# Performance work log

Hardware: AMD Instinct MI355X
Metric: run time of the kernel (lower is better)

The kernel has to match this reference:

```python
import jax, jax.numpy as jnp
import numpy as np

BS, SEQ, D_MODEL = 4, 1024, 4096
N_Q_HEADS, N_KV_HEADS, D_K, D_V = 32, 8, 128, 128
ROPE_BASE = 10000.0


def _rotate_half(x):
    x1, x2 = jnp.split(x, 2, axis=-1)
    return jnp.concatenate([-x2, x1], axis=-1)


def _apply_rope(x, pos0):
    # x: [bs, heads, seq, d]; positions pos0 .. pos0+seq-1
    d = x.shape[-1]
    seq = x.shape[2]
    inv_freq = 1.0 / (ROPE_BASE ** (jnp.arange(0, d, 2, dtype=jnp.float32) / d))  # [d/2]
    pos = (pos0 + jnp.arange(seq)).astype(jnp.float32)  # [seq]
    ang = pos[:, None] * inv_freq[None, :]  # [seq, d/2]
    cos = jnp.concatenate([jnp.cos(ang), jnp.cos(ang)], axis=-1)  # [seq, d]
    sin = jnp.concatenate([jnp.sin(ang), jnp.sin(ang)], axis=-1)
    return x * cos[None, None] + _rotate_half(x) * sin[None, None]


def setup_inputs() -> dict:
    key = jax.random.key(0)
    ks = jax.random.split(key, 8)
    w_scale = 0.02  # keep logits in a sane range (original uses raw normal init)
    return {
        "query": jax.random.normal(ks[0], (BS, SEQ, D_MODEL), dtype=jnp.float32),
        "key": jax.random.normal(ks[1], (BS, SEQ, D_MODEL), dtype=jnp.float32),
        "value": jax.random.normal(ks[2], (BS, SEQ, D_MODEL), dtype=jnp.float32),
        "mask": jnp.zeros((BS, SEQ, SEQ), dtype=jnp.float32),
        "wq": jax.random.normal(ks[3], (D_MODEL, N_Q_HEADS * D_K), dtype=jnp.float32) * w_scale,
        "wk": jax.random.normal(ks[4], (D_MODEL, N_KV_HEADS * D_K), dtype=jnp.float32) * w_scale,
        "wv": jax.random.normal(ks[5], (D_MODEL, N_KV_HEADS * D_V), dtype=jnp.float32) * w_scale,
        "wo": jax.random.normal(ks[6], (N_Q_HEADS * D_V, D_MODEL), dtype=jnp.float32) * w_scale,
        "curr_seq_pos": 0,
    }


def reference(query, key, value, mask, wq, wk, wv, wo, curr_seq_pos):
    bs, sq, _ = query.shape
    n_groups = N_Q_HEADS // N_KV_HEADS
    # projections -> [bs, heads, seq, d]
    q = (query @ wq).reshape(bs, sq, N_Q_HEADS, D_K).transpose((0, 2, 1, 3))
    sk = key.shape[1]
    k = (key @ wk).reshape(bs, sk, N_KV_HEADS, 1, D_K)
    k = jnp.repeat(k, n_groups, axis=3).reshape(bs, sk, N_Q_HEADS, D_K).transpose((0, 2, 1, 3))
    v = (value @ wv).reshape(bs, sk, N_KV_HEADS, 1, D_V)
    v = jnp.repeat(v, n_groups, axis=3).reshape(bs, sk, N_Q_HEADS, D_V).transpose((0, 2, 1, 3))
    scale = jnp.sqrt(jnp.float32(D_K))
    q = _apply_rope(q, curr_seq_pos)
    k = _apply_rope(k, curr_seq_pos)
    # [bs, h, sq, sk]
    raw = jnp.einsum("bhqd,bhkd->bhqk", q, k) / scale
    masked = raw + mask[:bs, None, curr_seq_pos:curr_seq_pos + sq, :sk]
    attn = jax.nn.softmax(masked, axis=-1)
    out = jnp.einsum("bhqk,bhkd->bhqd", attn, v)
    out = out.transpose((0, 2, 1, 3)).reshape(bs, sq, N_Q_HEADS * D_V)
    return out @ wo
```

## Files before the change

### kernel.cpp

```cpp
#include <hip/hip_runtime.h>


using ushort = unsigned short;
typedef __attribute__((ext_vector_type(8))) short short8;
typedef __attribute__((ext_vector_type(4))) short short4v;
typedef __attribute__((ext_vector_type(4))) float f32x4;
typedef __attribute__((ext_vector_type(4))) unsigned int uint4v;

__device__ __forceinline__ ushort f2bf(float x) {
  unsigned int u = __float_as_uint(x);
  u += 0x7FFFu + ((u >> 16) & 1u);
  return (ushort)(u >> 16);
}
__device__ __forceinline__ float bf2f(ushort h) {
  return __uint_as_float(((unsigned int)h) << 16);
}
__device__ __forceinline__ unsigned int cvt_pk_bf16(float lo, float hi) {
  unsigned int r;
  asm("v_cvt_pk_bf16_f32 %0, %1, %2" : "=v"(r) : "v"(lo), "v"(hi));
  return r;
}

__device__ __forceinline__ void async_copy16(const void* g, void* l) {
  __builtin_amdgcn_global_load_lds((const __attribute__((address_space(1))) void*)g,
                                   (__attribute__((address_space(3))) void*)l, 16, 0, 0);
}

__global__ __launch_bounds__(256)
void cvt_f32_bf16(const float* __restrict__ in, ushort* __restrict__ out, int n4) {
  const int i = blockIdx.x * 256 + threadIdx.x;
  if (i < n4) {
    const float4 f = ((const float4*)in)[i];
    short4v v;
    v[0] = (short)f2bf(f.x); v[1] = (short)f2bf(f.y);
    v[2] = (short)f2bf(f.z); v[3] = (short)f2bf(f.w);
    ((short4v*)out)[i] = v;
  }
}

__global__ __launch_bounds__(256)
void transpose_cvt(const float* __restrict__ B, ushort* __restrict__ Bt, int N) {
  __shared__ ushort t[64][72];
  const int n0 = blockIdx.x * 64, k0 = blockIdx.y * 64;
  const int tid = threadIdx.x;
  const int r = tid >> 3, c8 = (tid & 7) * 8;
#pragma unroll
  for (int p = 0; p < 2; p++) {
    const float* src = B + (size_t)(k0 + r + p * 32) * N + n0 + c8;
    const float4 f0 = *(const float4*)src;
    const float4 f1 = *(const float4*)(src + 4);
    ushort* d = &t[r + p * 32][c8];
    d[0] = f2bf(f0.x); d[1] = f2bf(f0.y); d[2] = f2bf(f0.z); d[3] = f2bf(f0.w);
    d[4] = f2bf(f1.x); d[5] = f2bf(f1.y); d[6] = f2bf(f1.z); d[7] = f2bf(f1.w);
  }
  __syncthreads();
#pragma unroll
  for (int p = 0; p < 2; p++) {
    const int n = r + p * 32;
    short8 o;
#pragma unroll
    for (int j = 0; j < 8; j++) o[j] = (short)t[c8 + j][n];
    *(short8*)(Bt + (size_t)(n0 + n) * 4096 + k0 + c8) = o;
  }
}

template <int MODE, bool AF32>
__global__ __launch_bounds__(256, 2)
void gemm_bt(const float* __restrict__ Af, const float* __restrict__ A2f,
             const ushort* __restrict__ Abf, const ushort* __restrict__ Bt,
             ushort* __restrict__ C, ushort* __restrict__ C2,
             float* __restrict__ Cf, const int* __restrict__ posp,
             int N, float scale) {
  constexpr int K = 4096;
  __shared__ alignas(16) ushort As[128 * 32];
  __shared__ alignas(16) ushort Bs[128 * 32];
  const int tid = threadIdx.x;
  const int wave = tid >> 6, lane = tid & 63;
  const int quad = lane >> 4, l16 = lane & 15;
  const int m0 = blockIdx.y * 128, n0 = blockIdx.x * 128;
  const int wm = (wave & 1) * 64, wn2 = (wave >> 1) * 32;

  const size_t aoff = (size_t)(m0 + wave * 16 + (lane >> 2)) * K + (lane & 3) * 8;
  const float* gAf = nullptr;
  const ushort* gAb = nullptr;
  if constexpr (AF32) {
    const float* Ause = Af;
    if constexpr (MODE == 4) {
      if (n0 >= 1024) Ause = A2f;
    }
    gAf = Ause + aoff;
  } else {
    gAb = Abf + aoff;
  }
  const ushort* gB = Bt + (size_t)(n0 + wave * 16 + (lane >> 2)) * K + (lane & 3) * 8;
  ushort* lA = As + wave * 512;
  ushort* lB = Bs + wave * 512;
  constexpr size_t rstep = (size_t)64 * K;

  f32x4 acc[4][4] = {};

  for (int kt = 0; kt < K; kt += 32) {
    if constexpr (AF32) {
      const float4 a0 = *(const float4*)(gAf + kt);
      const float4 a1 = *(const float4*)(gAf + kt + 4);
      const float4 b0 = *(const float4*)(gAf + rstep + kt);
      const float4 b1 = *(const float4*)(gAf + rstep + kt + 4);
      uint4v v0, v1;
      v0[0] = cvt_pk_bf16(a0.x, a0.y); v0[1] = cvt_pk_bf16(a0.z, a0.w);
      v0[2] = cvt_pk_bf16(a1.x, a1.y); v0[3] = cvt_pk_bf16(a1.z, a1.w);
      v1[0] = cvt_pk_bf16(b0.x, b0.y); v1[1] = cvt_pk_bf16(b0.z, b0.w);
      v1[2] = cvt_pk_bf16(b1.x, b1.y); v1[3] = cvt_pk_bf16(b1.z, b1.w);
      *(uint4v*)(lA + lane * 8) = v0;
      *(uint4v*)(lA + 2048 + lane * 8) = v1;
    } else {
      async_copy16(gAb + kt, lA);
      async_copy16(gAb + rstep + kt, lA + 2048);
    }
    async_copy16(gB + kt, lB);
    async_copy16(gB + rstep + kt, lB + 2048);
    __syncthreads();
    short8 af[4], bfrag[4];
#pragma unroll
    for (int i = 0; i < 4; i++) {
      af[i] = *(const short8*)(As + (wm + i * 16 + l16) * 32 + quad * 8);
      bfrag[i] = *(const short8*)(
          Bs + (wn2 + (i & 1) * 16 + (i >> 1) * 64 + l16) * 32 + quad * 8);
    }
#pragma unroll
    for (int i = 0; i < 4; i++)
#pragma unroll
      for (int j = 0; j < 4; j++)
        acc[i][j] = __builtin_amdgcn_mfma_f32_16x16x32_bf16(af[i], bfrag[j],
                                                            acc[i][j], 0, 0, 0);
    __syncthreads();
  }

  if constexpr (MODE == 0) {
#pragma unroll
    for (int i = 0; i < 4; i++)
#pragma unroll
      for (int j = 0; j < 4; j++) {
        const int n = n0 + wn2 + (j & 1) * 16 + (j >> 1) * 64 + l16;
        const int mb = m0 + wm + i * 16 + quad * 4;
#pragma unroll
        for (int r = 0; r < 4; r++)
          Cf[(size_t)(mb + r) * N + n] = acc[i][j][r] * scale;
      }
  } else {
    const bool kv_v = (MODE == 4) && (n0 >= 1024);
    if (!kv_v) {
      const int pos0 = posp[0];
      const int h = (MODE == 1) ? (n0 >> 7) : (n0 >> 7);
      const int NH = (MODE == 1) ? 32 : 8;
      constexpr float lgbase = -0.20762050593045983f;
      float invf[2];
      invf[0] = exp2f((float)(wn2 + l16) * lgbase);
      invf[1] = exp2f((float)(wn2 + 16 + l16) * lgbase);
#pragma unroll
      for (int i = 0; i < 4; i++) {
#pragma unroll
        for (int r = 0; r < 4; r++) {
          const int m = m0 + wm + i * 16 + quad * 4 + r;
          const int s = m & 1023, bb = m >> 10;
          const float p = (float)(s + pos0);
          ushort* row = C + (((size_t)bb * NH + h) * 1024 + s) * 128;
#pragma unroll
          for (int jj = 0; jj < 2; jj++) {
            float sn, cs;
            sincosf(p * invf[jj], &sn, &cs);
            const float x1 = acc[i][jj][r] * scale;
            const float x2 = acc[i][jj + 2][r] * scale;
            const int dlo = wn2 + jj * 16 + l16;
            row[dlo] = f2bf(x1 * cs - x2 * sn);
            row[dlo + 64] = f2bf(x2 * cs + x1 * sn);
          }
        }
      }
    } else {
      const int hh = (n0 - 1024) >> 7;
#pragma unroll
      for (int i = 0; i < 4; i++)
#pragma unroll
        for (int j = 0; j < 4; j++) {
          const int d = wn2 + (j & 1) * 16 + (j >> 1) * 64 + l16;
          const int mb = m0 + wm + i * 16 + quad * 4;
#pragma unroll
          for (int r = 0; r < 4; r++) {
            const int m = mb + r;
            const int bb = m >> 10, s = m & 1023;
            C2[(((size_t)bb * 8 + hh) * 128 + d) * 1024 + s] = f2bf(acc[i][j][r]);
          }
        }
    }
  }
}

__global__ __launch_bounds__(256, 2)
void attn_kernel(const ushort* __restrict__ Qh, const ushort* __restrict__ Kh,
                 const ushort* __restrict__ Vt, const ushort* __restrict__ Mk,
                 ushort* __restrict__ Oh) {
  __shared__ alignas(16) ushort smem[36864];
  ushort* const Ks0 = smem;
  ushort* const Ks1 = smem + 8192;
  ushort* const Vs0 = smem + 16384;
  ushort* const Vs1 = smem + 24576;
  ushort* const Ps = smem + 32768;
  ushort* const Qtmp = smem + 16384;

  int bid = (blockIdx.z * 32 + blockIdx.y) * 16 + blockIdx.x;
  bid = (bid & 7) * 256 + (bid >> 3);
  const int b = bid >> 9, h = (bid >> 4) & 31;
  const int q0 = (bid & 15) * 64;
  const int hkv = h >> 2;
  const int tid = threadIdx.x;
  const int wave = tid >> 6, lane = tid & 63;
  const int quad = lane >> 4, l16 = lane & 15;
  const int vr = lane >> 3;
  const int vkc = (lane & 7) ^ (vr & 7);

  const ushort* Qg = Qh + (((size_t)b * 32 + h) * 1024 + q0) * 128;
  const ushort* Kg = Kh + ((size_t)b * 8 + hkv) * (size_t)(1024 * 128);
  const ushort* Vg = Vt + ((size_t)b * 8 + hkv) * (size_t)(128 * 1024);
  const ushort* Mg = Mk + ((size_t)b * 1024 + q0) * 1024;

#pragma unroll
  for (int c = 0; c < 4; c++) {
    const int i = wave * 4 + c;
    const int row = i * 4 + quad;
    const int kc = l16 ^ (c * 4 + quad);
    async_copy16(Qg + (size_t)row * 128 + kc * 8, Qtmp + i * 512);
  }
#pragma unroll
  for (int c = 0; c < 4; c++) {
    const int i = wave * 4 + c;
    const int row = i * 4 + quad;
    const int kc = l16 ^ (c * 4 + quad);
    async_copy16(Kg + (size_t)row * 128 + kc * 8, Ks0 + i * 512);
  }
  __asm__ volatile("s_waitcnt vmcnt(0)" ::: "memory");
  short8 qreg[4];
#pragma unroll
  for (int ks = 0; ks < 4; ks++)
    qreg[ks] = *(const short8*)(Qtmp + (size_t)(wave * 16 + l16) * 128 +
                                (((ks * 4 + quad) ^ l16) * 8));
  __syncthreads();
#pragma unroll
  for (int c = 0; c < 4; c++) {
    const int i = wave * 4 + c;
    async_copy16(Vg + (size_t)(i * 8 + vr) * 1024 + vkc * 8, Vs0 + i * 512);
  }

  float m_i[4], l_p[4];
#pragma unroll
  for (int r = 0; r < 4; r++) { m_i[r] = -1e30f; l_p[r] = 0.0f; }
  f32x4 acc[8] = {};

  ushort* const PW = Ps + wave * 1024;

  for (int kt = 0; kt < 1024; kt += 64) {
    const int it = kt >> 6;
    ushort* const Kc = (it & 1) ? Ks1 : Ks0;
    ushort* const Vc = (it & 1) ? Vs1 : Vs0;
    ushort* const Kn = (it & 1) ? Ks0 : Ks1;
    ushort* const Vn = (it & 1) ? Vs0 : Vs1;
    __syncthreads();

    ushort mr[4][4];
#pragma unroll
    for (int nt = 0; nt < 4; nt++)
#pragma unroll
      for (int r = 0; r < 4; r++)
        mr[nt][r] = Mg[(size_t)(wave * 16 + quad * 4 + r) * 1024 +
                       kt + nt * 16 + l16];

    f32x4 s[4] = {};
    __builtin_amdgcn_s_setprio(1);
#pragma unroll
    for (int ks = 0; ks < 4; ks++) {
      const int ko = ((ks * 4 + quad) ^ l16) * 8;
#pragma unroll
      for (int nt = 0; nt < 4; nt++) {
        const short8 bk = *(const short8*)(Kc + (size_t)(nt * 16 + l16) * 128 + ko);
        s[nt] = __builtin_amdgcn_mfma_f32_16x16x32_bf16(qreg[ks], bk, s[nt], 0, 0, 0);
      }
    }
    __builtin_amdgcn_s_setprio(0);

    if (kt < 960) {
#pragma unroll
      for (int c = 0; c < 4; c++) {
        const int i = wave * 4 + c;
        const int row = i * 4 + quad;
        const int kc = l16 ^ (c * 4 + quad);
        async_copy16(Kg + (size_t)(kt + 64 + row) * 128 + kc * 8, Kn + i * 512);
      }
#pragma unroll
      for (int c = 0; c < 4; c++) {
        const int i = wave * 4 + c;
        async_copy16(Vg + (size_t)(i * 8 + vr) * 1024 + kt + 64 + vkc * 8, Vn + i * 512);
      }
    }

#pragma unroll
    for (int nt = 0; nt < 4; nt++)
#pragma unroll
      for (int r = 0; r < 4; r++) s[nt][r] += bf2f(mr[nt][r]);

    float mx[4];
    int need = 0;
#pragma unroll
    for (int r = 0; r < 4; r++) {
      float v = fmaxf(fmaxf(s[0][r], s[1][r]), fmaxf(s[2][r], s[3][r]));
#pragma unroll
      for (int off = 1; off < 16; off <<= 1) v = fmaxf(v, __shfl_xor(v, off));
      mx[r] = v;
      need |= (v > m_i[r] + 8.0f) ? 1 : 0;
    }
    if (__any(need)) {
#pragma unroll
      for (int r = 0; r < 4; r++) {
        const float mnew = fmaxf(m_i[r], mx[r]);
        const float al = __expf(m_i[r] - mnew);
        m_i[r] = mnew;
        l_p[r] *= al;
#pragma unroll
        for (int dt = 0; dt < 8; dt++) acc[dt][r] *= al;
      }
    }

#pragma unroll
    for (int r = 0; r < 4; r++) {
      const int prow = quad * 4 + r;
      const int key8 = ((prow >> 1) & 7) * 8;
      const float p0 = __expf(s[0][r] - m_i[r]);
      const float p1 = __expf(s[1][r] - m_i[r]);
      const float p2 = __expf(s[2][r] - m_i[r]);
      const float p3 = __expf(s[3][r] - m_i[r]);
      l_p[r] += (p0 + p1) + (p2 + p3);
      const unsigned int u01 = cvt_pk_bf16(p0, p1);
      const unsigned int u23 = cvt_pk_bf16(p2, p3);
      ushort* row = PW + prow * 64;
      row[l16 ^ key8] = (ushort)u01;
      row[(16 + l16) ^ key8] = (ushort)(u01 >> 16);
      row[(32 + l16) ^ key8] = (ushort)u23;
      row[(48 + l16) ^ key8] = (ushort)(u23 >> 16);
    }
    __asm__ volatile("s_waitcnt lgkmcnt(0)" ::: "memory");

    __builtin_amdgcn_s_setprio(1);
#pragma unroll
    for (int kk = 0; kk < 2; kk++) {
      const int pslot = ((kk * 4 + quad) ^ (l16 >> 1)) * 8;
      const short8 ap = *(const short8*)(PW + (size_t)l16 * 64 + pslot);
#pragma unroll
      for (int dt = 0; dt < 8; dt++) {
        const int vo = ((kk * 4 + quad) ^ (l16 & 7)) * 8;
        const short8 bv = *(const short8*)(Vc + (size_t)(dt * 16 + l16) * 64 + vo);
        acc[dt] = __builtin_amdgcn_mfma_f32_16x16x32_bf16(ap, bv, acc[dt], 0, 0, 0);
      }
    }
    __builtin_amdgcn_s_setprio(0);
  }

  ushort* Og = Oh + ((size_t)b * 1024 + q0 + wave * 16) * 4096 + h * 128;
#pragma unroll
  for (int r = 0; r < 4; r++) {
    float l = l_p[r];
#pragma unroll
    for (int off = 1; off < 16; off <<= 1) l += __shfl_xor(l, off);
    const float inv = 1.0f / l;
#pragma unroll
    for (int dt = 0; dt < 8; dt++)
      Og[(size_t)(quad * 4 + r) * 4096 + dt * 16 + l16] = f2bf(acc[dt][r] * inv);
  }
}

extern "C" void kernel_launch(void* const* d_in, const int* in_sizes, int n_in,
                              void* d_out, int out_size, void* d_ws, size_t ws_size,
                              hipStream_t stream) {
  (void)in_sizes; (void)n_in; (void)out_size; (void)ws_size;
  const float* query = (const float*)d_in[0];
  const float* key = (const float*)d_in[1];
  const float* value = (const float*)d_in[2];
  const float* mask = (const float*)d_in[3];
  const float* wq = (const float*)d_in[4];
  const float* wk = (const float*)d_in[5];
  const float* wv = (const float*)d_in[6];
  const float* wo = (const float*)d_in[7];
  const int* pos = (const int*)d_in[8];
  float* out = (float*)d_out;

  char* ws = (char*)d_ws;
  const size_t MB = 1024 * 1024;
  ushort* qb = (ushort*)(ws + 0 * MB);
  ushort* Khb = (ushort*)(ws + 0 * MB);
  ushort* Vtb = (ushort*)(ws + 8 * MB);
  ushort* wqT = (ushort*)(ws + 32 * MB);
  ushort* wkvT = (ushort*)(ws + 32 * MB);
  ushort* Ohb = (ushort*)(ws + 32 * MB);
  ushort* Qhb = (ushort*)(ws + 64 * MB);
  ushort* woT = (ushort*)(ws + 64 * MB);
  ushort* mbf = (ushort*)(ws + 96 * MB);

  dim3 blk(256);
  cvt_f32_bf16<<<dim3(4096), blk, 0, stream>>>(mask, mbf, 1048576);
  cvt_f32_bf16<<<dim3(16384), blk, 0, stream>>>(query, qb, 4194304);

  transpose_cvt<<<dim3(64, 64), blk, 0, stream>>>(wq, wqT, 4096);
  gemm_bt<1, false><<<dim3(32, 32), blk, 0, stream>>>(
      nullptr, nullptr, qb, wqT, Qhb, nullptr, nullptr, pos, 4096,
      0.08838834764831845f);

  transpose_cvt<<<dim3(16, 64), blk, 0, stream>>>(wk, wkvT, 1024);
  transpose_cvt<<<dim3(16, 64), blk, 0, stream>>>(wv, wkvT + (size_t)1024 * 4096, 1024);
  gemm_bt<4, true><<<dim3(16, 32), blk, 0, stream>>>(
      key, value, nullptr, wkvT, Khb, Vtb, nullptr, pos, 2048, 1.0f);

  attn_kernel<<<dim3(16, 32, 4), blk, 0, stream>>>(Qhb, Khb, Vtb, mbf, Ohb);

  transpose_cvt<<<dim3(64, 64), blk, 0, stream>>>(wo, woT, 4096);
  gemm_bt<0, false><<<dim3(32, 32), blk, 0, stream>>>(
      nullptr, nullptr, Ohb, woT, nullptr, nullptr, out, pos, 4096, 1.0f);
}
```

Before: 936.5 us.

## Double-buffer GEMM LDS tiles to overlap next-tile loads with MFMA

Converts the projection GEMM's shared-memory A/B tiles into two ping-pong buffers. The next k-tile's async copies, and for fp32 inputs its register loads plus bf16 conversion, are issued before the current tile's MFMAs, which cuts one barrier per iteration and hides global-load latency. Wave priority is also raised around the MFMA block. The cost is double the LDS use (32 KB per block) and more live registers in the fp32 path, which could pressure occupancy at the two-blocks-per-CU launch bound.

```diff
diff --git a/kernel.cpp b/kernel.cpp
--- a/kernel.cpp
+++ b/kernel.cpp
@@ -72,8 +72,8 @@
              float* __restrict__ Cf, const int* __restrict__ posp,
              int N, float scale) {
   constexpr int K = 4096;
-  __shared__ alignas(16) ushort As[128 * 32];
-  __shared__ alignas(16) ushort Bs[128 * 32];
+  __shared__ alignas(16) ushort As[2][128 * 32];
+  __shared__ alignas(16) ushort Bs[2][128 * 32];
   const int tid = threadIdx.x;
   const int wave = tid >> 6, lane = tid & 63;
   const int quad = lane >> 4, l16 = lane & 15;
@@ -93,46 +93,82 @@
     gAb = Abf + aoff;
   }
   const ushort* gB = Bt + (size_t)(n0 + wave * 16 + (lane >> 2)) * K + (lane & 3) * 8;
-  ushort* lA = As + wave * 512;
-  ushort* lB = Bs + wave * 512;
+  const int woff = wave * 512;
   constexpr size_t rstep = (size_t)64 * K;
 
   f32x4 acc[4][4] = {};
 
+  if constexpr (AF32) {
+    const float4 a0 = *(const float4*)(gAf);
+    const float4 a1 = *(const float4*)(gAf + 4);
+    const float4 b0 = *(const float4*)(gAf + rstep);
+    const float4 b1 = *(const float4*)(gAf + rstep + 4);
+    uint4v v0, v1;
+    v0[0] = cvt_pk_bf16(a0.x, a0.y); v0[1] = cvt_pk_bf16(a0.z, a0.w);
+    v0[2] = cvt_pk_bf16(a1.x, a1.y); v0[3] = cvt_pk_bf16(a1.z, a1.w);
+    v1[0] = cvt_pk_bf16(b0.x, b0.y); v1[1] = cvt_pk_bf16(b0.z, b0.w);
+    v1[2] = cvt_pk_bf16(b1.x, b1.y); v1[3] = cvt_pk_bf16(b1.z, b1.w);
+    *(uint4v*)(As[0] + woff + lane * 8) = v0;
+    *(uint4v*)(As[0] + 2048 + woff + lane * 8) = v1;
+  } else {
+    async_copy16(gAb, As[0] + woff);
+    async_copy16(gAb + rstep, As[0] + 2048 + woff);
+  }
+  async_copy16(gB, Bs[0] + woff);
+  async_copy16(gB + rstep, Bs[0] + 2048 + woff);
+
   for (int kt = 0; kt < K; kt += 32) {
+    const int cur = (kt >> 5) & 1;
+    const int nxt = cur ^ 1;
+    const bool pf = (kt + 32) < K;
+    __syncthreads();
+
+    float4 a0, a1, b0, b1;
     if constexpr (AF32) {
-      const float4 a0 = *(const float4*)(gAf + kt);
-      const float4 a1 = *(const float4*)(gAf + kt + 4);
-      const float4 b0 = *(const float4*)(gAf + rstep + kt);
-      const float4 b1 = *(const float4*)(gAf + rstep + kt + 4);
-      uint4v v0, v1;
-      v0[0] = cvt_pk_bf16(a0.x, a0.y); v0[1] = cvt_pk_bf16(a0.z, a0.w);
-      v0[2] = cvt_pk_bf16(a1.x, a1.y); v0[3] = cvt_pk_bf16(a1.z, a1.w);
-      v1[0] = cvt_pk_bf16(b0.x, b0.y); v1[1] = cvt_pk_bf16(b0.z, b0.w);
-      v1[2] = cvt_pk_bf16(b1.x, b1.y); v1[3] = cvt_pk_bf16(b1.z, b1.w);
-      *(uint4v*)(lA + lane * 8) = v0;
-      *(uint4v*)(lA + 2048 + lane * 8) = v1;
+      if (pf) {
+        a0 = *(const float4*)(gAf + kt + 32);
+        a1 = *(const float4*)(gAf + kt + 36);
+        b0 = *(const float4*)(gAf + rstep + kt + 32);
+        b1 = *(const float4*)(gAf + rstep + kt + 36);
+      }
     } else {
-      async_copy16(gAb + kt, lA);
-      async_copy16(gAb + rstep + kt, lA + 2048);
-    }
-    async_copy16(gB + kt, lB);
-    async_copy16(gB + rstep + kt, lB + 2048);
-    __syncthreads();
+      if (pf) {
+        async_copy16(gAb + kt + 32, As[nxt] + woff);
+        async_copy16(gAb + rstep + kt + 32, As[nxt] + 2048 + woff);
+      }
+    }
+    if (pf) {
+      async_copy16(gB + kt + 32, Bs[nxt] + woff);
+      async_copy16(gB + rstep + kt + 32, Bs[nxt] + 2048 + woff);
+    }
+
     short8 af[4], bfrag[4];
 #pragma unroll
     for (int i = 0; i < 4; i++) {
-      af[i] = *(const short8*)(As + (wm + i * 16 + l16) * 32 + quad * 8);
+      af[i] = *(const short8*)(As[cur] + (wm + i * 16 + l16) * 32 + quad * 8);
       bfrag[i] = *(const short8*)(
-          Bs + (wn2 + (i & 1) * 16 + (i >> 1) * 64 + l16) * 32 + quad * 8);
-    }
+          Bs[cur] + (wn2 + (i & 1) * 16 + (i >> 1) * 64 + l16) * 32 + quad * 8);
+    }
+    __builtin_amdgcn_s_setprio(1);
 #pragma unroll
     for (int i = 0; i < 4; i++)
 #pragma unroll
       for (int j = 0; j < 4; j++)
         acc[i][j] = __builtin_amdgcn_mfma_f32_16x16x32_bf16(af[i], bfrag[j],
                                                             acc[i][j], 0, 0, 0);
-    __syncthreads();
+    __builtin_amdgcn_s_setprio(0);
+
+    if constexpr (AF32) {
+      if (pf) {
+        uint4v v0, v1;
+        v0[0] = cvt_pk_bf16(a0.x, a0.y); v0[1] = cvt_pk_bf16(a0.z, a0.w);
+        v0[2] = cvt_pk_bf16(a1.x, a1.y); v0[3] = cvt_pk_bf16(a1.z, a1.w);
+        v1[0] = cvt_pk_bf16(b0.x, b0.y); v1[1] = cvt_pk_bf16(b0.z, b0.w);
+        v1[2] = cvt_pk_bf16(b1.x, b1.y); v1[3] = cvt_pk_bf16(b1.z, b1.w);
+        *(uint4v*)(As[nxt] + woff + lane * 8) = v0;
+        *(uint4v*)(As[nxt] + 2048 + woff + lane * 8) = v1;
+      }
+    }
   }
 
   if constexpr (MODE == 0) {
```

Result: no change. 932.7 us (-0.4%).
